# Performance work log

Hardware: AMD Instinct MI355X
Metric: run time of the kernel (lower is better)

## Reference

```python
import jax, jax.numpy as jnp
import numpy as np
import math

B, S, D = 2, 2048, 1024
H, DK, DV = 16, 64, 64  # head_count, query_size, value_size; H*DV == D
NEG_INF = -jnp.inf


def setup_inputs() -> dict:
    key = jax.random.key(0)
    ks = jax.random.split(key, 10)
    sc = 0.02
    return {
        "input": jax.random.normal(ks[0], (B, S, D), dtype=jnp.float32),
        "padding_mask": jnp.zeros((B, S), dtype=jnp.float32),  # 0 = valid, 1 = padded
        "wq_w": jax.random.normal(ks[1], (H * DK, D), dtype=jnp.float32) * sc,
        "wq_b": jnp.zeros((H * DK,), dtype=jnp.float32),
        "wk_w": jax.random.normal(ks[2], (H * DK, D), dtype=jnp.float32) * sc,
        "wk_b": jnp.zeros((H * DK,), dtype=jnp.float32),
        "wv_w": jax.random.normal(ks[3], (H * DV, D), dtype=jnp.float32) * sc,
        "wv_b": jnp.zeros((H * DV,), dtype=jnp.float32),
        "fin_w": jax.random.normal(ks[4], (D, H * DV), dtype=jnp.float32) * sc,
        "fin_b": jnp.zeros((D,), dtype=jnp.float32),
    }


def reference(input, padding_mask, wq_w, wq_b, wk_w, wk_b, wv_w, wv_b, fin_w, fin_b):
    b, s, _ = input.shape
    # projections -> [b, h, s, d]
    Q = (input @ wq_w.T + wq_b).reshape(b, s, H, DK).transpose(0, 2, 1, 3)
    K = (input @ wk_w.T + wk_b).reshape(b, s, H, DK).transpose(0, 2, 1, 3)
    V = (input @ wv_w.T + wv_b).reshape(b, s, H, DV).transpose(0, 2, 1, 3)

    # padding mask: pad*(-inf), nan_to_num(0*inf -> 0); broadcast over query dim
    pad = jnp.where(padding_mask > 0, NEG_INF, 0.0)[:, None, None, :]  # [b,1,1,s]
    i = jnp.arange(s)
    causal = jnp.where(i[None, :] < i[:, None] + 1, 0.0, NEG_INF)  # [s,s]
    mask = pad + causal[None, None, :, :]

    # (QK^T + mask) / sqrt(dk), softmax over keys
    logits = (jnp.einsum("bhqd,bhkd->bhqk", Q, K) + mask) / math.sqrt(DK)
    attn = jax.nn.softmax(logits, axis=-1)
    out = jnp.einsum("bhqk,bhkd->bqhd", attn, V).reshape(b, s, H * DV)
    return out @ fin_w.T + fin_b
```

## Files before the change

### kernel.cpp

```cpp
#include <hip/hip_runtime.h>


typedef __bf16 bf16;
typedef __bf16 bf16x4 __attribute__((ext_vector_type(4)));
typedef __bf16 bf16x8 __attribute__((ext_vector_type(8)));
typedef float  f32x4  __attribute__((ext_vector_type(4)));

#define B_  2
#define S_  2048
#define D_  1024
#define H_  16
#define HD  64
#define NEG_BIG (-3.0e38f)
#define SCALE_LOG2E 0.1803368801111204f

__device__ __forceinline__ void lds16(const void* g, void* l) {
    __builtin_amdgcn_global_load_lds((const __attribute__((address_space(1))) void*)g,
                                     (__attribute__((address_space(3))) void*)l, 16, 0, 0);
}

__device__ __forceinline__ f32x4 mfma16(bf16x8 a, bf16x8 b, f32x4 c) {
    return __builtin_amdgcn_mfma_f32_16x16x32_bf16(a, b, c, 0, 0, 0);
}

__global__ __launch_bounds__(256) void convert_k(const float* __restrict__ X,
                                                 const float* __restrict__ wq,
                                                 const float* __restrict__ wk,
                                                 const float* __restrict__ wv,
                                                 const float* __restrict__ wo,
                                                 bf16* __restrict__ dst) {
    const int gid = blockIdx.x * 256 + threadIdx.x;
    const int i   = gid * 4;
    const float* src;
    int off;
    if      (i < (4 << 20)) { src = X;  off = 0; }
    else if (i < (5 << 20)) { src = wq; off = 4 << 20; }
    else if (i < (6 << 20)) { src = wk; off = 5 << 20; }
    else if (i < (7 << 20)) { src = wv; off = 6 << 20; }
    else                    { src = wo; off = 7 << 20; }
    const float4 v = *(const float4*)(src + (i - off));
    bf16x4 p;
    p[0] = (bf16)v.x; p[1] = (bf16)v.y; p[2] = (bf16)v.z; p[3] = (bf16)v.w;
    *(bf16x4*)(dst + i) = p;
}

__global__ __launch_bounds__(256) void gemm_qkv(const bf16* __restrict__ A,
                                                const bf16* __restrict__ Wq,
                                                const bf16* __restrict__ Wk,
                                                const bf16* __restrict__ Wv,
                                                const float* __restrict__ bq,
                                                const float* __restrict__ bk,
                                                const float* __restrict__ bv,
                                                bf16* __restrict__ Qw,
                                                bf16* __restrict__ Kw,
                                                bf16* __restrict__ Vw) {
    constexpr int K = 1024;
    __shared__ bf16 sA[128 * 32];
    __shared__ bf16 sB[128 * 32];
    const int tid  = threadIdx.x;
    const int l15  = tid & 15;
    const int quad = (tid & 63) >> 4;
    const int wid  = tid >> 6;
    const int seg  = blockIdx.x >> 3;
    const int bn   = blockIdx.x & 7;
    const int bm   = blockIdx.y;
    const int wm   = (wid >> 1) * 64;
    const int wn   = (wid & 1) * 64;

    const bf16* W    = (seg == 0) ? Wq : (seg == 1) ? Wk : Wv;
    const float* bias = (seg == 0) ? bq : (seg == 1) ? bk : bv;

    const bf16* Ab = A + (size_t)bm * 128 * K;
    const bf16* Wb = W + (size_t)bn * 128 * K;

    f32x4 acc[4][4] = {};

    for (int k0 = 0; k0 < K; k0 += 32) {
        __syncthreads();
        #pragma unroll
        for (int it = 0; it < 2; ++it) {
            int c = it * 256 + tid;
            int row = c >> 2, c8 = c & 3;
            lds16(Ab + row * K + k0 + c8 * 8, (char*)sA + c * 16);
            lds16(Wb + row * K + k0 + c8 * 8, (char*)sB + c * 16);
        }
        __syncthreads();
        bf16x8 af[4], bfr[4];
        #pragma unroll
        for (int i = 0; i < 4; ++i)
            af[i] = *(const bf16x8*)&sA[(wm + i * 16 + l15) * 32 + quad * 8];
        #pragma unroll
        for (int i = 0; i < 4; ++i)
            bfr[i] = *(const bf16x8*)&sB[(wn + i * 16 + l15) * 32 + quad * 8];
        #pragma unroll
        for (int mi = 0; mi < 4; ++mi)
            #pragma unroll
            for (int ni = 0; ni < 4; ++ni)
                acc[mi][ni] = mfma16(af[mi], bfr[ni], acc[mi][ni]);
    }

    #pragma unroll
    for (int ni = 0; ni < 4; ++ni) {
        const int n  = bn * 128 + wn + ni * 16 + l15;
        const float bv_ = bias[n];
        const int h = n >> 6;
        #pragma unroll
        for (int mi = 0; mi < 4; ++mi) {
            const int m0 = bm * 128 + wm + mi * 16 + quad * 4;
            if (seg == 2) {
                const int dv = n & 63;
                const int b = m0 >> 11, s = m0 & 2047;
                bf16x4 pack;
                #pragma unroll
                for (int r = 0; r < 4; ++r) pack[r] = (bf16)(acc[mi][ni][r] + bv_);
                *(bf16x4*)&Vw[(((size_t)(b * H_ + h) * HD + dv) << 11) + s] = pack;
            } else {
                bf16* C = (seg == 0) ? Qw : Kw;
                const float qs = (seg == 0) ? SCALE_LOG2E : 1.0f;
                const int dk = n & 63;
                #pragma unroll
                for (int r = 0; r < 4; ++r) {
                    const int m = m0 + r, b = m >> 11, s = m & 2047;
                    C[(((size_t)(b * H_ + h) << 11) + s) * HD + dk] =
                        (bf16)((acc[mi][ni][r] + bv_) * qs);
                }
            }
        }
    }
}

__global__ __launch_bounds__(256) void gemm_fin(const bf16* __restrict__ A,
                                                const bf16* __restrict__ W,
                                                const float* __restrict__ bias,
                                                float* __restrict__ C) {
    constexpr int N = 1024, K = 1024;
    __shared__ bf16 sA[64 * 32];
    __shared__ bf16 sB[128 * 32];
    const int tid  = threadIdx.x;
    const int l15  = tid & 15;
    const int quad = (tid & 63) >> 4;
    const int wid  = tid >> 6;
    const int bm   = blockIdx.x >> 3;
    const int bn   = blockIdx.x & 7;
    const int wm   = (wid & 1) * 32;
    const int wn   = (wid >> 1) * 64;

    const bf16* Ab = A + (size_t)bm * 64 * K;
    const bf16* Wb = W + (size_t)bn * 128 * K;

    f32x4 acc[2][4] = {};

    for (int k0 = 0; k0 < K; k0 += 32) {
        __syncthreads();
        {
            int c = tid, row = c >> 2, c8 = c & 3;
            lds16(Ab + row * K + k0 + c8 * 8, (char*)sA + c * 16);
        }
        #pragma unroll
        for (int it = 0; it < 2; ++it) {
            int c = it * 256 + tid;
            int row = c >> 2, c8 = c & 3;
            lds16(Wb + row * K + k0 + c8 * 8, (char*)sB + c * 16);
        }
        __syncthreads();
        bf16x8 af[2], bfr[4];
        #pragma unroll
        for (int i = 0; i < 2; ++i)
            af[i] = *(const bf16x8*)&sA[(wm + i * 16 + l15) * 32 + quad * 8];
        #pragma unroll
        for (int i = 0; i < 4; ++i)
            bfr[i] = *(const bf16x8*)&sB[(wn + i * 16 + l15) * 32 + quad * 8];
        #pragma unroll
        for (int mi = 0; mi < 2; ++mi)
            #pragma unroll
            for (int ni = 0; ni < 4; ++ni)
                acc[mi][ni] = mfma16(af[mi], bfr[ni], acc[mi][ni]);
    }

    #pragma unroll
    for (int ni = 0; ni < 4; ++ni) {
        const int n  = bn * 128 + wn + ni * 16 + l15;
        const float bv = bias[n];
        #pragma unroll
        for (int mi = 0; mi < 2; ++mi) {
            const int m0 = bm * 64 + wm + mi * 16 + quad * 4;
            #pragma unroll
            for (int r = 0; r < 4; ++r)
                C[(size_t)(m0 + r) * N + n] = acc[mi][ni][r] + bv;
        }
    }
}

__global__ __launch_bounds__(256, 2) void attn_k(const bf16* __restrict__ Q,
                                                 const bf16* __restrict__ K,
                                                 const bf16* __restrict__ Vt,
                                                 const float* __restrict__ pmask,
                                                 bf16* __restrict__ Aout) {
    __shared__ bf16 sK_[2 * 128 * 32];
    __shared__ bf16 sV[4 * 64 * 32];
    __shared__ bf16 sP[4096];
    const int tid  = threadIdx.x;
    const int l15  = tid & 15;
    const int quad = (tid & 63) >> 4;
    const int wid  = tid >> 6;
    const int j    = blockIdx.x >> 5;
    const int bh   = blockIdx.x & 31;
    const int b    = bh >> 4;
    const int h    = bh & 15;
    const int a_  = j >> 3, bq_ = j & 7;
    const int qt  = (a_ == 0) ? (31 - bq_) : (a_ == 1) ? bq_
                  : (a_ == 2) ? (23 - bq_) : (8 + bq_);
    const int nkt = (qt >> 1) + 1;

    const bf16* Qg = Q + ((size_t)bh * S_ + qt * 64) * HD;
    #pragma unroll
    for (int it = 0; it < 2; ++it) {
        int c = it * 256 + tid;
        int pl = c >> 8, row = (c >> 2) & 63, c8 = c & 3;
        lds16(Qg + row * HD + pl * 32 + c8 * 8, (char*)sK_ + c * 16);
    }
    const bf16* Kg = K  + (size_t)bh * S_ * HD;
    const bf16* Vg = Vt + (size_t)bh * HD * S_;
    __syncthreads();
    bf16x8 aq[2];
    #pragma unroll
    for (int kk = 0; kk < 2; ++kk)
        aq[kk] = *(const bf16x8*)&sK_[(kk * 64 + wid * 16 + l15) * 32 + quad * 8];

    bf16x8 onesv;
    #pragma unroll
    for (int i = 0; i < 8; ++i) onesv[i] = (bf16)1.0f;

    f32x4 lacc = {};
    f32x4 o[4] = {};
    const int qrow = wid * 16 + quad * 4;
    const int qg0  = qt * 64 + qrow;

    for (int kt = 0; kt < nkt; ++kt) {
        __syncthreads();
        #pragma unroll
        for (int it = 0; it < 4; ++it) {
            int c = it * 256 + tid;
            { int pl = c >> 9, row = (c >> 2) & 127, c8 = c & 3;
              lds16(Kg + (size_t)kt * 128 * HD + row * HD + pl * 32 + c8 * 8,
                    (char*)sK_ + c * 16); }
            { int kc = c >> 8, dv = (c >> 2) & 63, c8 = c & 3;
              lds16(Vg + kt * 128 + dv * S_ + kc * 32 + c8 * 8,
                    (char*)sV + c * 16); }
        }
        __syncthreads();

        f32x4 s[8] = {};
        #pragma unroll
        for (int tc = 0; tc < 8; ++tc)
            #pragma unroll
            for (int kk = 0; kk < 2; ++kk) {
                bf16x8 bk = *(const bf16x8*)
                    &sK_[(kk * 128 + tc * 16 + l15) * 32 + quad * 8];
                s[tc] = mfma16(aq[kk], bk, s[tc]);
            }

        float pmadd[8];
        #pragma unroll
        for (int tc = 0; tc < 8; ++tc) {
            int kg = kt * 128 + tc * 16 + l15;
            pmadd[tc] = (pmask[b * S_ + kg] > 0.f) ? NEG_BIG : 0.f;
        }
        const bool lastt = (kt == nkt - 1);
        #pragma unroll
        for (int tc = 0; tc < 8; ++tc)
            #pragma unroll
            for (int r = 0; r < 4; ++r) {
                float v = s[tc][r] + pmadd[tc];
                if (lastt && (kt * 128 + tc * 16 + l15 > qg0 + r)) v = NEG_BIG;
                s[tc][r] = exp2f(v);
            }

        #pragma unroll
        for (int hf = 0; hf < 2; ++hf) {
            #pragma unroll
            for (int tc4 = 0; tc4 < 4; ++tc4) {
                const int tc   = hf * 4 + tc4;
                const int keyh = tc4 * 16 + l15;
                const int c    = keyh >> 3;
                const int sub  = keyh & 7;
                #pragma unroll
                for (int r = 0; r < 4; ++r) {
                    const int q  = qrow + r;
                    const int cs = c ^ ((q >> 1) & 7);
                    sP[q * 64 + cs * 8 + sub] = (bf16)s[tc][r];
                }
            }
            #pragma unroll
            for (int c2 = 0; c2 < 2; ++c2) {
                const int qr = wid * 16 + l15;
                const int cs = (c2 * 4 + quad) ^ ((qr >> 1) & 7);
                bf16x8 ap = *(const bf16x8*)&sP[qr * 64 + cs * 8];
                const int kc = hf * 2 + c2;
                lacc = mfma16(ap, onesv, lacc);
                #pragma unroll
                for (int vc = 0; vc < 4; ++vc) {
                    bf16x8 bv = *(const bf16x8*)
                        &sV[(kc * 64 + vc * 16 + l15) * 32 + quad * 8];
                    o[vc] = mfma16(ap, bv, o[vc]);
                }
            }
        }
    }

    #pragma unroll
    for (int r = 0; r < 4; ++r) {
        float inv = 1.f / lacc[r];
        size_t base = ((size_t)b * S_ + qg0 + r) * D_ + h * HD;
        #pragma unroll
        for (int vc = 0; vc < 4; ++vc)
            Aout[base + vc * 16 + l15] = (bf16)(o[vc][r] * inv);
    }
}

extern "C" void kernel_launch(void* const* d_in, const int* in_sizes, int n_in,
                              void* d_out, int out_size, void* d_ws, size_t ws_size,
                              hipStream_t stream) {
    const float* X   = (const float*)d_in[0];
    const float* pm  = (const float*)d_in[1];
    const float* wq  = (const float*)d_in[2];
    const float* bq  = (const float*)d_in[3];
    const float* wk  = (const float*)d_in[4];
    const float* bk  = (const float*)d_in[5];
    const float* wv  = (const float*)d_in[6];
    const float* bvb = (const float*)d_in[7];
    const float* wo  = (const float*)d_in[8];
    const float* bo  = (const float*)d_in[9];
    float* out = (float*)d_out;

    char* ws = (char*)d_ws;
    bf16* Xb  = (bf16*)(ws);
    bf16* Wqb = (bf16*)(ws + (8u  << 20));
    bf16* Wkb = (bf16*)(ws + (10u << 20));
    bf16* Wvb = (bf16*)(ws + (12u << 20));
    bf16* Wob = (bf16*)(ws + (14u << 20));
    bf16* Qw  = (bf16*)(ws + (16u << 20));
    bf16* Kw  = (bf16*)(ws + (24u << 20));
    bf16* Vw  = (bf16*)(ws + (32u << 20));
    bf16* Aw  = (bf16*)(ws + (40u << 20));

    convert_k<<<dim3(8192), dim3(256), 0, stream>>>(X, wq, wk, wv, wo, Xb);
    gemm_qkv<<<dim3(24, 32), dim3(256), 0, stream>>>(Xb, Wqb, Wkb, Wvb,
                                                     bq, bk, bvb, Qw, Kw, Vw);
    attn_k<<<dim3(1024), dim3(256), 0, stream>>>(Qw, Kw, Vw, pm, Aw);
    gemm_fin<<<dim3(512), dim3(256), 0, stream>>>(Aw, Wob, bo, out);
}
```

Baseline: 193.1 us.

## Split attention keys across warps with register-resident operands and LDS reduction

The attention kernel now splits each 128-key tile across the four warps (32 keys each) instead of splitting query rows. Each warp keeps all 64 queries' Q fragments in registers, loads K and V directly from global memory into registers with double-buffered K prefetch, and computes S^T so the exp'd probabilities feed the PV MFMA without an LDS round trip. Per-block tile staging and barriers are removed. The cost is a final cross-warp reduction of partial O and row sums through a large fp32 LDS buffer, plus higher register pressure from the 16 output accumulators, which may lower occupancy.

```diff
diff --git a/kernel.cpp b/kernel.cpp
--- a/kernel.cpp
+++ b/kernel.cpp
@@ -196,9 +196,8 @@
                                                  const bf16* __restrict__ Vt,
                                                  const float* __restrict__ pmask,
                                                  bf16* __restrict__ Aout) {
-    __shared__ bf16 sK_[2 * 128 * 32];
-    __shared__ bf16 sV[4 * 64 * 32];
-    __shared__ bf16 sP[4096];
+    __shared__ float sO[4 * 64 * 65];
+    __shared__ float sL[4 * 64];
     const int tid  = threadIdx.x;
     const int l15  = tid & 15;
     const int quad = (tid & 63) >> 4;
@@ -212,109 +211,133 @@
                   : (a_ == 2) ? (23 - bq_) : (8 + bq_);
     const int nkt = (qt >> 1) + 1;
 
-    const bf16* Qg = Q + ((size_t)bh * S_ + qt * 64) * HD;
-    #pragma unroll
-    for (int it = 0; it < 2; ++it) {
-        int c = it * 256 + tid;
-        int pl = c >> 8, row = (c >> 2) & 63, c8 = c & 3;
-        lds16(Qg + row * HD + pl * 32 + c8 * 8, (char*)sK_ + c * 16);
-    }
+    const bf16* Qg = Q  + ((size_t)bh * S_ + qt * 64) * HD;
     const bf16* Kg = K  + (size_t)bh * S_ * HD;
     const bf16* Vg = Vt + (size_t)bh * HD * S_;
+
+    bf16x8 qb[4][2];
+    #pragma unroll
+    for (int qf = 0; qf < 4; ++qf)
+        #pragma unroll
+        for (int kk = 0; kk < 2; ++kk)
+            qb[qf][kk] = *(const bf16x8*)&Qg[(qf * 16 + l15) * HD + kk * 32 + quad * 8];
+
+    const int krow0 = (l15 >> 2) * 8 + (l15 & 3);
+    const int wkey  = wid * 32;
+
+    bf16x8 onesv;
+    #pragma unroll
+    for (int i = 0; i < 8; ++i) onesv[i] = (bf16)1.0f;
+
+    f32x4 o[4][4] = {};
+    f32x4 lacc[4] = {};
+
+    bf16x8 kaA[2][2], kaB[2][2];
+    #pragma unroll
+    for (int f = 0; f < 2; ++f)
+        #pragma unroll
+        for (int kk = 0; kk < 2; ++kk)
+            kaA[f][kk] = *(const bf16x8*)
+                &Kg[(size_t)(wkey + krow0 + f * 4) * HD + kk * 32 + quad * 8];
+
+#define TILE(KC, KN, KT)                                                        \
+  {                                                                             \
+    const int kb = (KT) * 128 + wkey;                                           \
+    const bool lastt = ((KT) == nkt - 1);                                       \
+    bf16x8 va[4];                                                               \
+    _Pragma("unroll")                                                           \
+    for (int dvf = 0; dvf < 4; ++dvf)                                           \
+        va[dvf] = *(const bf16x8*)                                              \
+            &Vg[(size_t)(dvf * 16 + l15) * S_ + kb + quad * 8];                 \
+    f32x4 s[2][4] = {};                                                         \
+    _Pragma("unroll")                                                           \
+    for (int f = 0; f < 2; ++f)                                                 \
+        _Pragma("unroll")                                                       \
+        for (int qf = 0; qf < 4; ++qf) {                                        \
+            s[f][qf] = mfma16(KC[f][0], qb[qf][0], s[f][qf]);                   \
+            s[f][qf] = mfma16(KC[f][1], qb[qf][1], s[f][qf]);                   \
+        }                                                                       \
+    if ((KT) + 1 < nkt) {                                                       \
+        const int kb2 = ((KT) + 1) * 128 + wkey;                                \
+        _Pragma("unroll")                                                       \
+        for (int f = 0; f < 2; ++f)                                             \
+            _Pragma("unroll")                                                   \
+            for (int kk = 0; kk < 2; ++kk)                                      \
+                KN[f][kk] = *(const bf16x8*)                                    \
+                    &Kg[(size_t)(kb2 + krow0 + f * 4) * HD + kk * 32 + quad * 8]; \
+    }                                                                           \
+    float pmadd[8];                                                             \
+    _Pragma("unroll")                                                           \
+    for (int f = 0; f < 2; ++f)                                                 \
+        _Pragma("unroll")                                                       \
+        for (int r = 0; r < 4; ++r)                                             \
+            pmadd[f * 4 + r] =                                                  \
+                (pmask[b * S_ + kb + quad * 8 + f * 4 + r] > 0.f) ? NEG_BIG : 0.f; \
+    _Pragma("unroll")                                                           \
+    for (int qf = 0; qf < 4; ++qf) {                                            \
+        const int qg = qt * 64 + qf * 16 + l15;                                 \
+        bf16x8 pb;                                                              \
+        _Pragma("unroll")                                                       \
+        for (int f = 0; f < 2; ++f)                                             \
+            _Pragma("unroll")                                                   \
+            for (int r = 0; r < 4; ++r) {                                       \
+                float v = s[f][qf][r] + pmadd[f * 4 + r];                       \
+                if (lastt && (kb + quad * 8 + f * 4 + r > qg)) v = NEG_BIG;     \
+                pb[f * 4 + r] = (bf16)exp2f(v);                                 \
+            }                                                                   \
+        lacc[qf] = mfma16(onesv, pb, lacc[qf]);                                 \
+        _Pragma("unroll")                                                       \
+        for (int dvf = 0; dvf < 4; ++dvf)                                       \
+            o[dvf][qf] = mfma16(va[dvf], pb, o[dvf][qf]);                       \
+    }                                                                           \
+  }
+
+    int kt = 0;
+    for (;;) {
+        TILE(kaA, kaB, kt); if (++kt == nkt) break;
+        TILE(kaB, kaA, kt); if (++kt == nkt) break;
+    }
+#undef TILE
+
+    {
+        float* sOw = sO + wid * (64 * 65);
+        #pragma unroll
+        for (int dvf = 0; dvf < 4; ++dvf)
+            #pragma unroll
+            for (int qf = 0; qf < 4; ++qf)
+                #pragma unroll
+                for (int r = 0; r < 4; ++r)
+                    sOw[(dvf * 16 + quad * 4 + r) * 65 + qf * 16 + l15] = o[dvf][qf][r];
+        if (quad == 0) {
+            #pragma unroll
+            for (int qf = 0; qf < 4; ++qf)
+                sL[wid * 64 + qf * 16 + l15] = lacc[qf][0];
+        }
+    }
     __syncthreads();
-    bf16x8 aq[2];
-    #pragma unroll
-    for (int kk = 0; kk < 2; ++kk)
-        aq[kk] = *(const bf16x8*)&sK_[(kk * 64 + wid * 16 + l15) * 32 + quad * 8];
-
-    bf16x8 onesv;
-    #pragma unroll
-    for (int i = 0; i < 8; ++i) onesv[i] = (bf16)1.0f;
-
-    f32x4 lacc = {};
-    f32x4 o[4] = {};
-    const int qrow = wid * 16 + quad * 4;
-    const int qg0  = qt * 64 + qrow;
-
-    for (int kt = 0; kt < nkt; ++kt) {
-        __syncthreads();
-        #pragma unroll
-        for (int it = 0; it < 4; ++it) {
-            int c = it * 256 + tid;
-            { int pl = c >> 9, row = (c >> 2) & 127, c8 = c & 3;
-              lds16(Kg + (size_t)kt * 128 * HD + row * HD + pl * 32 + c8 * 8,
-                    (char*)sK_ + c * 16); }
-            { int kc = c >> 8, dv = (c >> 2) & 63, c8 = c & 3;
-              lds16(Vg + kt * 128 + dv * S_ + kc * 32 + c8 * 8,
-                    (char*)sV + c * 16); }
-        }
-        __syncthreads();
-
-        f32x4 s[8] = {};
-        #pragma unroll
-        for (int tc = 0; tc < 8; ++tc)
-            #pragma unroll
-            for (int kk = 0; kk < 2; ++kk) {
-                bf16x8 bk = *(const bf16x8*)
-                    &sK_[(kk * 128 + tc * 16 + l15) * 32 + quad * 8];
-                s[tc] = mfma16(aq[kk], bk, s[tc]);
-            }
-
-        float pmadd[8];
-        #pragma unroll
-        for (int tc = 0; tc < 8; ++tc) {
-            int kg = kt * 128 + tc * 16 + l15;
-            pmadd[tc] = (pmask[b * S_ + kg] > 0.f) ? NEG_BIG : 0.f;
-        }
-        const bool lastt = (kt == nkt - 1);
-        #pragma unroll
-        for (int tc = 0; tc < 8; ++tc)
-            #pragma unroll
-            for (int r = 0; r < 4; ++r) {
-                float v = s[tc][r] + pmadd[tc];
-                if (lastt && (kt * 128 + tc * 16 + l15 > qg0 + r)) v = NEG_BIG;
-                s[tc][r] = exp2f(v);
-            }
-
-        #pragma unroll
-        for (int hf = 0; hf < 2; ++hf) {
-            #pragma unroll
-            for (int tc4 = 0; tc4 < 4; ++tc4) {
-                const int tc   = hf * 4 + tc4;
-                const int keyh = tc4 * 16 + l15;
-                const int c    = keyh >> 3;
-                const int sub  = keyh & 7;
-                #pragma unroll
-                for (int r = 0; r < 4; ++r) {
-                    const int q  = qrow + r;
-                    const int cs = c ^ ((q >> 1) & 7);
-                    sP[q * 64 + cs * 8 + sub] = (bf16)s[tc][r];
-                }
-            }
-            #pragma unroll
-            for (int c2 = 0; c2 < 2; ++c2) {
-                const int qr = wid * 16 + l15;
-                const int cs = (c2 * 4 + quad) ^ ((qr >> 1) & 7);
-                bf16x8 ap = *(const bf16x8*)&sP[qr * 64 + cs * 8];
-                const int kc = hf * 2 + c2;
-                lacc = mfma16(ap, onesv, lacc);
-                #pragma unroll
-                for (int vc = 0; vc < 4; ++vc) {
-                    bf16x8 bv = *(const bf16x8*)
-                        &sV[(kc * 64 + vc * 16 + l15) * 32 + quad * 8];
-                    o[vc] = mfma16(ap, bv, o[vc]);
-                }
-            }
-        }
-    }
-
-    #pragma unroll
-    for (int r = 0; r < 4; ++r) {
-        float inv = 1.f / lacc[r];
-        size_t base = ((size_t)b * S_ + qg0 + r) * D_ + h * HD;
-        #pragma unroll
-        for (int vc = 0; vc < 4; ++vc)
-            Aout[base + vc * 16 + l15] = (bf16)(o[vc][r] * inv);
+    {
+        const int q   = tid >> 2;
+        const int dvg = (tid & 3) * 16;
+        const float l = sL[q] + sL[64 + q] + sL[128 + q] + sL[192 + q];
+        const float inv = 1.f / l;
+        bf16x8 p0, p1;
+        #pragma unroll
+        for (int i = 0; i < 8; ++i) {
+            const int dv = dvg + i;
+            float a = sO[dv * 65 + q] + sO[4160 + dv * 65 + q]
+                    + sO[8320 + dv * 65 + q] + sO[12480 + dv * 65 + q];
+            p0[i] = (bf16)(a * inv);
+        }
+        #pragma unroll
+        for (int i = 0; i < 8; ++i) {
+            const int dv = dvg + 8 + i;
+            float a = sO[dv * 65 + q] + sO[4160 + dv * 65 + q]
+                    + sO[8320 + dv * 65 + q] + sO[12480 + dv * 65 + q];
+            p1[i] = (bf16)(a * inv);
+        }
+        const size_t base = ((size_t)b * S_ + qt * 64 + q) * D_ + h * HD + dvg;
+        *(bf16x8*)&Aout[base]     = p0;
+        *(bf16x8*)&Aout[base + 8] = p1;
     }
 }
 
```

After: 216.6 us. +12.2%, slower.

## Compute transposed S^T in attention to keep P in registers, drop LDS staging

Applied to the files above, without the earlier changes.

The attention kernel now computes S^T = K·Q^T, so that each lane's MFMA output for the scores already sits in the B-operand layout needed for the P·V product. This removes the shared-memory sP staging buffer and its write/read round trip. Q is loaded straight from global memory into registers, and the padding mask is read with vector float4 loads. The output is stored as packed bf16x4. Lower LDS use together with launch_bounds raised to 4 is meant to improve occupancy, at the risk of register pressure or spills.

```diff
diff --git a/kernel.cpp b/kernel.cpp
--- a/kernel.cpp
+++ b/kernel.cpp
@@ -191,14 +191,13 @@
     }
 }
 
-__global__ __launch_bounds__(256, 2) void attn_k(const bf16* __restrict__ Q,
+__global__ __launch_bounds__(256, 4) void attn_k(const bf16* __restrict__ Q,
                                                  const bf16* __restrict__ K,
                                                  const bf16* __restrict__ Vt,
                                                  const float* __restrict__ pmask,
                                                  bf16* __restrict__ Aout) {
     __shared__ bf16 sK_[2 * 128 * 32];
     __shared__ bf16 sV[4 * 64 * 32];
-    __shared__ bf16 sP[4096];
     const int tid  = threadIdx.x;
     const int l15  = tid & 15;
     const int quad = (tid & 63) >> 4;
@@ -212,29 +211,24 @@
                   : (a_ == 2) ? (23 - bq_) : (8 + bq_);
     const int nkt = (qt >> 1) + 1;
 
-    const bf16* Qg = Q + ((size_t)bh * S_ + qt * 64) * HD;
-    #pragma unroll
-    for (int it = 0; it < 2; ++it) {
-        int c = it * 256 + tid;
-        int pl = c >> 8, row = (c >> 2) & 63, c8 = c & 3;
-        lds16(Qg + row * HD + pl * 32 + c8 * 8, (char*)sK_ + c * 16);
-    }
+    const bf16* Qg = Q  + ((size_t)bh * S_ + qt * 64) * HD;
     const bf16* Kg = K  + (size_t)bh * S_ * HD;
     const bf16* Vg = Vt + (size_t)bh * HD * S_;
-    __syncthreads();
-    bf16x8 aq[2];
+
+    bf16x8 qb[2];
     #pragma unroll
     for (int kk = 0; kk < 2; ++kk)
-        aq[kk] = *(const bf16x8*)&sK_[(kk * 64 + wid * 16 + l15) * 32 + quad * 8];
+        qb[kk] = *(const bf16x8*)&Qg[(wid * 16 + l15) * HD + kk * 32 + quad * 8];
+
+    const int krow0 = (l15 >> 2) * 8 + (l15 & 3);
+    const int qg    = qt * 64 + wid * 16 + l15;
 
     bf16x8 onesv;
     #pragma unroll
     for (int i = 0; i < 8; ++i) onesv[i] = (bf16)1.0f;
 
-    f32x4 lacc = {};
-    f32x4 o[4] = {};
-    const int qrow = wid * 16 + quad * 4;
-    const int qg0  = qt * 64 + qrow;
+    f32x4 o[4]  = {};
+    f32x4 lacc  = {};
 
     for (int kt = 0; kt < nkt; ++kt) {
         __syncthreads();
@@ -248,73 +242,57 @@
               lds16(Vg + kt * 128 + dv * S_ + kc * 32 + c8 * 8,
                     (char*)sV + c * 16); }
         }
-        __syncthreads();
-
-        f32x4 s[8] = {};
-        #pragma unroll
-        for (int tc = 0; tc < 8; ++tc)
-            #pragma unroll
-            for (int kk = 0; kk < 2; ++kk) {
-                bf16x8 bk = *(const bf16x8*)
-                    &sK_[(kk * 128 + tc * 16 + l15) * 32 + quad * 8];
-                s[tc] = mfma16(aq[kk], bk, s[tc]);
-            }
-
-        float pmadd[8];
-        #pragma unroll
-        for (int tc = 0; tc < 8; ++tc) {
-            int kg = kt * 128 + tc * 16 + l15;
-            pmadd[tc] = (pmask[b * S_ + kg] > 0.f) ? NEG_BIG : 0.f;
-        }
+        float4 pm4[8];
+        #pragma unroll
+        for (int g = 0; g < 4; ++g)
+            #pragma unroll
+            for (int f = 0; f < 2; ++f)
+                pm4[g * 2 + f] = *(const float4*)
+                    &pmask[b * S_ + kt * 128 + g * 32 + quad * 8 + f * 4];
+        __syncthreads();
+
         const bool lastt = (kt == nkt - 1);
         #pragma unroll
-        for (int tc = 0; tc < 8; ++tc)
-            #pragma unroll
-            for (int r = 0; r < 4; ++r) {
-                float v = s[tc][r] + pmadd[tc];
-                if (lastt && (kt * 128 + tc * 16 + l15 > qg0 + r)) v = NEG_BIG;
-                s[tc][r] = exp2f(v);
-            }
-
-        #pragma unroll
-        for (int hf = 0; hf < 2; ++hf) {
-            #pragma unroll
-            for (int tc4 = 0; tc4 < 4; ++tc4) {
-                const int tc   = hf * 4 + tc4;
-                const int keyh = tc4 * 16 + l15;
-                const int c    = keyh >> 3;
-                const int sub  = keyh & 7;
+        for (int g = 0; g < 4; ++g) {
+            f32x4 s[2] = {};
+            #pragma unroll
+            for (int f = 0; f < 2; ++f)
+                #pragma unroll
+                for (int kk = 0; kk < 2; ++kk) {
+                    bf16x8 ka = *(const bf16x8*)
+                        &sK_[(kk * 128 + g * 32 + krow0 + f * 4) * 32 + quad * 8];
+                    s[f] = mfma16(ka, qb[kk], s[f]);
+                }
+            bf16x8 pb;
+            #pragma unroll
+            for (int f = 0; f < 2; ++f) {
+                const float4 pmv = pm4[g * 2 + f];
                 #pragma unroll
                 for (int r = 0; r < 4; ++r) {
-                    const int q  = qrow + r;
-                    const int cs = c ^ ((q >> 1) & 7);
-                    sP[q * 64 + cs * 8 + sub] = (bf16)s[tc][r];
+                    float v = fmaf(((const float*)&pmv)[r], NEG_BIG, s[f][r]);
+                    if (lastt && (kt * 128 + g * 32 + quad * 8 + f * 4 + r > qg))
+                        v = NEG_BIG;
+                    pb[f * 4 + r] = (bf16)exp2f(v);
                 }
             }
-            #pragma unroll
-            for (int c2 = 0; c2 < 2; ++c2) {
-                const int qr = wid * 16 + l15;
-                const int cs = (c2 * 4 + quad) ^ ((qr >> 1) & 7);
-                bf16x8 ap = *(const bf16x8*)&sP[qr * 64 + cs * 8];
-                const int kc = hf * 2 + c2;
-                lacc = mfma16(ap, onesv, lacc);
-                #pragma unroll
-                for (int vc = 0; vc < 4; ++vc) {
-                    bf16x8 bv = *(const bf16x8*)
-                        &sV[(kc * 64 + vc * 16 + l15) * 32 + quad * 8];
-                    o[vc] = mfma16(ap, bv, o[vc]);
-                }
+            lacc = mfma16(onesv, pb, lacc);
+            #pragma unroll
+            for (int dvf = 0; dvf < 4; ++dvf) {
+                bf16x8 va = *(const bf16x8*)
+                    &sV[(g * 64 + dvf * 16 + l15) * 32 + quad * 8];
+                o[dvf] = mfma16(va, pb, o[dvf]);
             }
         }
     }
 
-    #pragma unroll
-    for (int r = 0; r < 4; ++r) {
-        float inv = 1.f / lacc[r];
-        size_t base = ((size_t)b * S_ + qg0 + r) * D_ + h * HD;
-        #pragma unroll
-        for (int vc = 0; vc < 4; ++vc)
-            Aout[base + vc * 16 + l15] = (bf16)(o[vc][r] * inv);
+    const float inv = 1.f / lacc[0];
+    const size_t base = ((size_t)b * S_ + qg) * D_ + h * HD + quad * 4;
+    #pragma unroll
+    for (int dvf = 0; dvf < 4; ++dvf) {
+        bf16x4 pack;
+        #pragma unroll
+        for (int r = 0; r < 4; ++r) pack[r] = (bf16)(o[dvf][r] * inv);
+        *(bf16x4*)&Aout[base + dvf * 16] = pack;
     }
 }
 
```

Result: no change. 189.7 us (-1.7%).
